# Kernel optimization log

Hardware: AMD Instinct MI355X
Metric: run time of the kernel (lower is better)

## Reference

```python
import jax, jax.numpy as jnp
import numpy as np

N = 30000      # num nodes (cells)
E = 480000     # num edges (avg degree 16)
D_IN = 1000    # input_dim (genes)
H = 8          # nheads
F_H = 32       # hidden_dim per head
D_EMB = 64     # embedding_dim
NEG_SLOPE = 0.2


def setup_inputs() -> dict:
    key = jax.random.key(0)
    ks = jax.random.split(key, 12)
    glorot = lambda k, shape, fan: (jax.random.normal(k, shape, jnp.float32)
                                    * (1.0 / np.sqrt(fan)))
    return {
        "x": jax.random.normal(ks[0], (N, D_IN), jnp.float32),
        "edge_index": jax.random.randint(ks[1], (2, E), 0, N),
        "edge_weight": jax.random.uniform(ks[2], (E,), jnp.float32),
        # GATConv params
        "W": glorot(ks[3], (D_IN, H * F_H), D_IN),
        "att_src": glorot(ks[4], (H, F_H), F_H),
        "att_dst": glorot(ks[5], (H, F_H), F_H),
        "bias_gat": jnp.zeros((H * F_H,), jnp.float32),
        # embedding Linear
        "emb_W": glorot(ks[6], (H * F_H, D_EMB), H * F_H),
        "emb_b": jnp.zeros((D_EMB,), jnp.float32),
        # decoder MLP
        "dec_W1": glorot(ks[7], (D_EMB, F_H), D_EMB),
        "dec_b1": jnp.zeros((F_H,), jnp.float32),
        "dec_W2": glorot(ks[8], (F_H, D_IN), F_H),
        "dec_b2": jnp.zeros((D_IN,), jnp.float32),
    }


def _gat_conv(x, edge_index, W, att_src, att_dst, bias):
    n = x.shape[0]
    h = (x @ W).reshape(n, H, F_H)                    # [N,H,F]
    a_s = jnp.einsum('nhf,hf->nh', h, att_src)        # [N,H]
    a_d = jnp.einsum('nhf,hf->nh', h, att_dst)        # [N,H]
    # add self loops (PyG default add_self_loops=True)
    loops = jnp.arange(n)
    src = jnp.concatenate([edge_index[0], loops])     # [E+N]
    dst = jnp.concatenate([edge_index[1], loops])     # [E+N]
    logits = jax.nn.leaky_relu(a_s[src] + a_d[dst], NEG_SLOPE)  # [E+N,H]
    # segment softmax over incoming edges of each destination node
    m = jax.ops.segment_max(logits, dst, num_segments=n)        # [N,H]
    p = jnp.exp(logits - m[dst])
    denom = jax.ops.segment_sum(p, dst, num_segments=n)         # [N,H]
    alpha = p / denom[dst]                                      # [E+N,H]
    msg = h[src] * alpha[:, :, None]                            # [E+N,H,F]
    out = jax.ops.segment_sum(msg, dst, num_segments=n)         # [N,H,F]
    return out.reshape(n, H * F_H) + bias


def reference(x, edge_index, edge_weight, W, att_src, att_dst, bias_gat,
              emb_W, emb_b, dec_W1, dec_b1, dec_W2, dec_b2):
    # edge_weight is accepted but unused: PyG GATConv with edge_dim=None has
    # no edge-feature pathway.
    h = jax.nn.relu(_gat_conv(x, edge_index, W, att_src, att_dst, bias_gat))
    z = h @ emb_W + emb_b                               # [N, D_EMB]
    d = jax.nn.relu(z @ dec_W1 + dec_b1)                # [N, F_H]
    recon = d @ dec_W2 + dec_b2                         # [N, D_IN]
    return recon, z
```

## Files before the change

### kernel.cpp

```cpp
#include <hip/hip_runtime.h>
#include <hip/hip_bf16.h>

#define N_NODES 30000
#define N_EDGES 480000
#define D_IN    1000
#define KPAD    1024
#define NHEAD   8
#define F_HID   32
#define D_EMB   64
#define NEG_SLOPE 0.2f
#define MAXDEG  64

typedef __attribute__((ext_vector_type(4))) float  f32x4;
typedef __attribute__((ext_vector_type(8))) __bf16 bf16x8;
typedef __attribute__((ext_vector_type(4))) __bf16 bf16x4;

#define WT_TOT    (256*KPAD + D_EMB*256 + F_HID*D_EMB + D_IN*F_HID)
#define WT_BLOCKS ((WT_TOT + 255) / 256)
#define ZC_BLOCKS ((N_NODES + 255) / 256)

__global__ __launch_bounds__(256) void cvt_w(
    const float* __restrict__ W, const float* __restrict__ emb_W,
    const float* __restrict__ d1, const float* __restrict__ d2,
    __bf16* __restrict__ WbT, __bf16* __restrict__ embT,
    __bf16* __restrict__ d1T, __bf16* __restrict__ d2T, int* __restrict__ cnt)
{
    int b = blockIdx.x;
    if (b < WT_BLOCKS) {
        int i = b * 256 + threadIdx.x;
        if (i < 256 * KPAD) {
            int n = i >> 10, k = i & 1023;
            WbT[i] = (k < D_IN) ? (__bf16)W[(size_t)k * 256 + n] : (__bf16)0.0f;
            return;
        }
        i -= 256 * KPAD;
        if (i < D_EMB * 256) {
            int n = i >> 8, k = i & 255;
            embT[i] = (__bf16)emb_W[(size_t)k * D_EMB + n];
            return;
        }
        i -= D_EMB * 256;
        if (i < F_HID * D_EMB) {
            int n = i >> 6, k = i & 63;
            d1T[i] = (__bf16)d1[(size_t)k * F_HID + n];
            return;
        }
        i -= F_HID * D_EMB;
        if (i < D_IN * F_HID) {
            int n = i >> 5, k = i & 31;
            d2T[i] = (__bf16)d2[(size_t)k * D_IN + n];
        }
        return;
    }
    b -= WT_BLOCKS;
    {
        int i = b * 256 + threadIdx.x;
        if (i < N_NODES) cnt[i] = 0;
    }
}

__device__ __forceinline__ void stage_tile(
    __bf16* lds, const __bf16* __restrict__ g, int base, int maxr,
    int K, int k0, int rows, int w, int lane)
{
    const int rsub = lane >> 2;
    const int c    = lane & 3;
    for (int off = w * 1024; off < rows * 64; off += 4096) {
        int r  = (off >> 6) + rsub;
        int gr = base + r; gr = gr > maxr ? maxr : gr;
        int chunk = c ^ (r & 3);
        const __bf16* gp = g + (size_t)gr * K + k0 + chunk * 8;
        __builtin_amdgcn_global_load_lds(
            (const __attribute__((address_space(1))) void*)gp,
            (__attribute__((address_space(3))) void*)((char*)lds + off),
            16, 0, 0);
    }
}

template<int BM, int BN, int RELU>
__global__ __launch_bounds__(256) void gemm_bf16(
    const __bf16* __restrict__ A, const __bf16* __restrict__ Bt,
    float* __restrict__ Cf, __bf16* __restrict__ Cb,
    const float* __restrict__ bias, int M, int Nn, int K)
{
    constexpr int MT = BM / 32;
    constexpr int NT = BN / 32;
    __shared__ __align__(16) __bf16 As[BM * 32];
    __shared__ __align__(16) __bf16 Bs[BN * 32];

    const int tid  = threadIdx.x;
    const int w    = tid >> 6, lane = tid & 63;
    const int wm   = w >> 1,   wn   = w & 1;
    const int quad = lane >> 4, l16 = lane & 15;
    const int bm = blockIdx.x * BM, bn = blockIdx.y * BN;

    f32x4 acc[MT][NT];
    #pragma unroll
    for (int i = 0; i < MT; i++)
        #pragma unroll
        for (int j = 0; j < NT; j++)
            acc[i][j] = (f32x4){0.f, 0.f, 0.f, 0.f};

    for (int k0 = 0; k0 < K; k0 += 32) {
        stage_tile(As, A,  bm, M  - 1, K, k0, BM, w, lane);
        stage_tile(Bs, Bt, bn, Nn - 1, K, k0, BN, w, lane);
        __syncthreads();

        bf16x8 af[MT], bfr[NT];
        #pragma unroll
        for (int mt = 0; mt < MT; mt++) {
            int r = wm * 64 + mt * 16 + l16;
            af[mt] = *(const bf16x8*)&As[r * 32 + (quad ^ (r & 3)) * 8];
        }
        #pragma unroll
        for (int nt = 0; nt < NT; nt++) {
            int r = wn * (NT * 16) + nt * 16 + l16;
            bfr[nt] = *(const bf16x8*)&Bs[r * 32 + (quad ^ (r & 3)) * 8];
        }
        #pragma unroll
        for (int mt = 0; mt < MT; mt++)
            #pragma unroll
            for (int nt = 0; nt < NT; nt++)
                acc[mt][nt] = __builtin_amdgcn_mfma_f32_16x16x32_bf16(
                    af[mt], bfr[nt], acc[mt][nt], 0, 0, 0);
        __syncthreads();
    }

    #pragma unroll
    for (int nt = 0; nt < NT; nt++) {
        int col = bn + wn * (NT * 16) + nt * 16 + l16;
        if (col >= Nn) continue;
        float bv = bias ? bias[col] : 0.0f;
        #pragma unroll
        for (int mt = 0; mt < MT; mt++) {
            int row0 = bm + wm * 64 + mt * 16 + quad * 4;
            #pragma unroll
            for (int rr = 0; rr < 4; rr++) {
                int row = row0 + rr;
                if (row < M) {
                    float v = acc[mt][nt][rr] + bv;
                    if (RELU) v = v > 0.f ? v : 0.f;
                    if (Cf) Cf[(size_t)row * Nn + col] = v;
                    if (Cb) Cb[(size_t)row * Nn + col] = (__bf16)v;
                }
            }
        }
    }
}

__device__ __forceinline__ void a_load_f32(
    const float* __restrict__ x, int bm, int M, int r0, int cb, f32x4* regs)
{
    if (cb < D_IN) {
        int g0 = bm + r0;      g0 = g0 > M - 1 ? M - 1 : g0;
        int g1 = bm + r0 + 64; g1 = g1 > M - 1 ? M - 1 : g1;
        const f32x4* p0 = (const f32x4*)(x + (size_t)g0 * D_IN + cb);
        const f32x4* p1 = (const f32x4*)(x + (size_t)g1 * D_IN + cb);
        regs[0] = p0[0]; regs[1] = p0[1];
        regs[2] = p1[0]; regs[3] = p1[1];
    } else {
        regs[0] = regs[1] = regs[2] = regs[3] = (f32x4){0.f, 0.f, 0.f, 0.f};
    }
}

__global__ __launch_bounds__(256, 1) void gemm1_fused(
    const float* __restrict__ x, const __bf16* __restrict__ WbT,
    __bf16* __restrict__ hb, int M)
{
    __shared__ __align__(16) __bf16 As[128 * 32];
    __shared__ __align__(16) __bf16 Bs[256 * 32];

    const int tid  = threadIdx.x;
    const int w    = tid >> 6, lane = tid & 63;
    const int wm   = w >> 1,   wn   = w & 1;
    const int quad = lane >> 4, l16 = lane & 15;
    const int bm   = blockIdx.x * 128;

    const int r0   = tid >> 2;
    const int cpos = tid & 3;
    const int cxor = (cpos ^ (r0 & 3)) << 3;

    f32x4 acc[4][8];
    #pragma unroll
    for (int i = 0; i < 4; i++)
        #pragma unroll
        for (int j = 0; j < 8; j++)
            acc[i][j] = (f32x4){0.f, 0.f, 0.f, 0.f};

    f32x4 ca[4], na[4];
    a_load_f32(x, bm, M, r0, cxor, ca);

    for (int k0 = 0; k0 < KPAD; k0 += 32) {
        a_load_f32(x, bm, M, r0, (k0 + 32) + cxor, na);
        stage_tile(Bs, WbT, 0, 255, KPAD, k0, 256, w, lane);
        {
            bf16x8 o;
            o[0]=(__bf16)ca[0].x; o[1]=(__bf16)ca[0].y; o[2]=(__bf16)ca[0].z; o[3]=(__bf16)ca[0].w;
            o[4]=(__bf16)ca[1].x; o[5]=(__bf16)ca[1].y; o[6]=(__bf16)ca[1].z; o[7]=(__bf16)ca[1].w;
            *(bf16x8*)&As[r0 * 32 + cpos * 8] = o;
            o[0]=(__bf16)ca[2].x; o[1]=(__bf16)ca[2].y; o[2]=(__bf16)ca[2].z; o[3]=(__bf16)ca[2].w;
            o[4]=(__bf16)ca[3].x; o[5]=(__bf16)ca[3].y; o[6]=(__bf16)ca[3].z; o[7]=(__bf16)ca[3].w;
            *(bf16x8*)&As[(r0 + 64) * 32 + cpos * 8] = o;
        }
        __syncthreads();

        bf16x8 af[4], bfr[8];
        #pragma unroll
        for (int mt = 0; mt < 4; mt++) {
            int r = wm * 64 + mt * 16 + l16;
            af[mt] = *(const bf16x8*)&As[r * 32 + (quad ^ (r & 3)) * 8];
        }
        #pragma unroll
        for (int nt = 0; nt < 8; nt++) {
            int r = wn * 128 + nt * 16 + l16;
            bfr[nt] = *(const bf16x8*)&Bs[r * 32 + (quad ^ (r & 3)) * 8];
        }
        #pragma unroll
        for (int mt = 0; mt < 4; mt++)
            #pragma unroll
            for (int nt = 0; nt < 8; nt++)
                acc[mt][nt] = __builtin_amdgcn_mfma_f32_16x16x32_bf16(
                    af[mt], bfr[nt], acc[mt][nt], 0, 0, 0);
        __syncthreads();

        #pragma unroll
        for (int i = 0; i < 4; i++) ca[i] = na[i];
    }

    #pragma unroll
    for (int nt = 0; nt < 8; nt++) {
        int col = wn * 128 + nt * 16 + l16;
        #pragma unroll
        for (int mt = 0; mt < 4; mt++) {
            int row0 = bm + wm * 64 + mt * 16 + quad * 4;
            #pragma unroll
            for (int rr = 0; rr < 4; rr++) {
                int row = row0 + rr;
                if (row < M)
                    hb[(size_t)row * 256 + col] = (__bf16)acc[mt][nt][rr];
            }
        }
    }
}

#define ATT_BLOCKS ((N_NODES * NHEAD + 255) / 256)
#define SC_BLOCKS  ((N_EDGES + 255) / 256)

__global__ __launch_bounds__(256) void att_scatter(
    const __bf16* __restrict__ hb, const float* __restrict__ att_src,
    const float* __restrict__ att_dst, const int* __restrict__ eidx,
    float* __restrict__ a_s, float* __restrict__ a_d,
    int* __restrict__ cnt, int* __restrict__ slots)
{
    int b = blockIdx.x;
    if (b < ATT_BLOCKS) {
        int i = b * 256 + threadIdx.x;
        if (i >= N_NODES * NHEAD) return;
        int hh = i & 7;
        const bf16x8* hp = (const bf16x8*)(hb + (size_t)i * F_HID);
        const float* sp = att_src + hh * F_HID;
        const float* dp = att_dst + hh * F_HID;
        float s = 0.f, d = 0.f;
        #pragma unroll
        for (int j = 0; j < 4; j++) {
            bf16x8 hv = hp[j];
            #pragma unroll
            for (int t = 0; t < 8; t++) {
                float f = (float)hv[t];
                s += f * sp[j * 8 + t];
                d += f * dp[j * 8 + t];
            }
        }
        a_s[i] = s;
        a_d[i] = d;
        return;
    }
    b -= ATT_BLOCKS;
    {
        int e = b * 256 + threadIdx.x;
        if (e < N_EDGES) {
            int d = eidx[N_EDGES + e];
            int slot = atomicAdd(&cnt[d], 1);
            slots[d * MAXDEG + slot] = eidx[e];
        }
    }
}

__device__ __forceinline__ float leaky(float x) {
    return x > 0.f ? x : NEG_SLOPE * x;
}

__global__ __launch_bounds__(256) void gat_aggregate(
    const __bf16* __restrict__ hb, const float* __restrict__ a_s,
    const float* __restrict__ a_d, const int* __restrict__ cnt,
    const int* __restrict__ slots, const float* __restrict__ bias,
    __bf16* __restrict__ hgatb)
{
    const int wid  = threadIdx.x >> 6;
    const int lane = threadIdx.x & 63;
    const int n = blockIdx.x * 4 + wid;
    if (n >= N_NODES) return;

    const int hh = lane >> 3;
    const int fo = (lane & 7) * 4;
    const int base = n * MAXDEG;
    const int c = cnt[n];
    const float adn = a_d[n * NHEAD + hh];

    float p = __expf(leaky(a_s[n * NHEAD + hh] + adn));
    float denom = p;
    f32x4 acc;
    {
        bf16x4 hv = *(const bf16x4*)(hb + (size_t)n * 256 + hh * F_HID + fo);
        acc.x = p * (float)hv[0]; acc.y = p * (float)hv[1];
        acc.z = p * (float)hv[2]; acc.w = p * (float)hv[3];
    }
    int e = 0;
    for (; e + 4 <= c; e += 4) {
        int s0 = slots[base + e + 0];
        int s1 = slots[base + e + 1];
        int s2 = slots[base + e + 2];
        int s3 = slots[base + e + 3];
        float l0 = a_s[s0 * NHEAD + hh], l1 = a_s[s1 * NHEAD + hh];
        float l2 = a_s[s2 * NHEAD + hh], l3 = a_s[s3 * NHEAD + hh];
        bf16x4 h0 = *(const bf16x4*)(hb + (size_t)s0 * 256 + hh * F_HID + fo);
        bf16x4 h1 = *(const bf16x4*)(hb + (size_t)s1 * 256 + hh * F_HID + fo);
        bf16x4 h2 = *(const bf16x4*)(hb + (size_t)s2 * 256 + hh * F_HID + fo);
        bf16x4 h3 = *(const bf16x4*)(hb + (size_t)s3 * 256 + hh * F_HID + fo);
        float p0 = __expf(leaky(l0 + adn)), p1 = __expf(leaky(l1 + adn));
        float p2 = __expf(leaky(l2 + adn)), p3 = __expf(leaky(l3 + adn));
        denom += (p0 + p1) + (p2 + p3);
        acc.x += p0*(float)h0[0] + p1*(float)h1[0] + p2*(float)h2[0] + p3*(float)h3[0];
        acc.y += p0*(float)h0[1] + p1*(float)h1[1] + p2*(float)h2[1] + p3*(float)h3[1];
        acc.z += p0*(float)h0[2] + p1*(float)h1[2] + p2*(float)h2[2] + p3*(float)h3[2];
        acc.w += p0*(float)h0[3] + p1*(float)h1[3] + p2*(float)h2[3] + p3*(float)h3[3];
    }
    for (; e < c; e++) {
        int s = slots[base + e];
        float pe = __expf(leaky(a_s[s * NHEAD + hh] + adn));
        denom += pe;
        bf16x4 hv = *(const bf16x4*)(hb + (size_t)s * 256 + hh * F_HID + fo);
        acc.x += pe * (float)hv[0]; acc.y += pe * (float)hv[1];
        acc.z += pe * (float)hv[2]; acc.w += pe * (float)hv[3];
    }
    float inv = 1.0f / denom;
    f32x4 bv = *(const f32x4*)(bias + lane * 4);
    float o0 = acc.x * inv + bv.x, o1 = acc.y * inv + bv.y;
    float o2 = acc.z * inv + bv.z, o3 = acc.w * inv + bv.w;
    o0 = o0 > 0.f ? o0 : 0.f;
    o1 = o1 > 0.f ? o1 : 0.f;
    o2 = o2 > 0.f ? o2 : 0.f;
    o3 = o3 > 0.f ? o3 : 0.f;
    bf16x4 ob;
    ob[0] = (__bf16)o0; ob[1] = (__bf16)o1; ob[2] = (__bf16)o2; ob[3] = (__bf16)o3;
    *(bf16x4*)(hgatb + (size_t)n * 256 + lane * 4) = ob;
}

__global__ __launch_bounds__(256) void gemm_zd(
    const __bf16* __restrict__ hgatb, const __bf16* __restrict__ embT,
    const __bf16* __restrict__ d1T, const float* __restrict__ emb_b,
    const float* __restrict__ dec_b1, float* __restrict__ z,
    __bf16* __restrict__ dbufb, int M)
{
    __shared__ __align__(16) __bf16 As[128 * 32];
    __shared__ __align__(16) __bf16 Bs[64 * 32];
    __shared__ __align__(16) __bf16 zS[128 * 64];
    __shared__ __align__(16) __bf16 Bs2[2 * 32 * 32];

    const int tid  = threadIdx.x;
    const int w    = tid >> 6, lane = tid & 63;
    const int wm   = w >> 1,   wn   = w & 1;
    const int quad = lane >> 4, l16 = lane & 15;
    const int bm = blockIdx.x * 128;

    stage_tile(Bs2,        d1T, 0, 31, 64, 0,  32, w, lane);
    stage_tile(Bs2 + 1024, d1T, 0, 31, 64, 32, 32, w, lane);

    f32x4 acc[4][2];
    #pragma unroll
    for (int i = 0; i < 4; i++) { acc[i][0] = (f32x4){0,0,0,0}; acc[i][1] = (f32x4){0,0,0,0}; }

    for (int k0 = 0; k0 < 256; k0 += 32) {
        stage_tile(As, hgatb, bm, M - 1, 256, k0, 128, w, lane);
        stage_tile(Bs, embT,  0,  D_EMB - 1, 256, k0, 64, w, lane);
        __syncthreads();
        bf16x8 af[4], bfr[2];
        #pragma unroll
        for (int mt = 0; mt < 4; mt++) {
            int r = wm * 64 + mt * 16 + l16;
            af[mt] = *(const bf16x8*)&As[r * 32 + (quad ^ (r & 3)) * 8];
        }
        #pragma unroll
        for (int nt = 0; nt < 2; nt++) {
            int r = wn * 32 + nt * 16 + l16;
            bfr[nt] = *(const bf16x8*)&Bs[r * 32 + (quad ^ (r & 3)) * 8];
        }
        #pragma unroll
        for (int mt = 0; mt < 4; mt++)
            #pragma unroll
            for (int nt = 0; nt < 2; nt++)
                acc[mt][nt] = __builtin_amdgcn_mfma_f32_16x16x32_bf16(
                    af[mt], bfr[nt], acc[mt][nt], 0, 0, 0);
        __syncthreads();
    }

    #pragma unroll
    for (int nt = 0; nt < 2; nt++) {
        int col = wn * 32 + nt * 16 + l16;
        float bv = emb_b[col];
        int t = col >> 5, cch = (col >> 3) & 3, j = col & 7;
        #pragma unroll
        for (int mt = 0; mt < 4; mt++) {
            int rl0 = wm * 64 + mt * 16 + quad * 4;
            #pragma unroll
            for (int rr = 0; rr < 4; rr++) {
                int rl = rl0 + rr;
                int row = bm + rl;
                float v = acc[mt][nt][rr] + bv;
                if (row < M) z[(size_t)row * D_EMB + col] = v;
                zS[t * 4096 + rl * 32 + (cch ^ (rl & 3)) * 8 + j] = (__bf16)v;
            }
        }
    }
    __syncthreads();

    f32x4 accd[4];
    #pragma unroll
    for (int i = 0; i < 4; i++) accd[i] = (f32x4){0,0,0,0};
    #pragma unroll
    for (int t = 0; t < 2; t++) {
        bf16x8 af[4], bfr;
        #pragma unroll
        for (int mt = 0; mt < 4; mt++) {
            int r = wm * 64 + mt * 16 + l16;
            af[mt] = *(const bf16x8*)&zS[t * 4096 + r * 32 + (quad ^ (r & 3)) * 8];
        }
        {
            int r = wn * 16 + l16;
            bfr = *(const bf16x8*)&Bs2[t * 1024 + r * 32 + (quad ^ (r & 3)) * 8];
        }
        #pragma unroll
        for (int mt = 0; mt < 4; mt++)
            accd[mt] = __builtin_amdgcn_mfma_f32_16x16x32_bf16(af[mt], bfr, accd[mt], 0, 0, 0);
    }
    {
        int col = wn * 16 + l16;
        float bv = dec_b1[col];
        #pragma unroll
        for (int mt = 0; mt < 4; mt++) {
            int rl0 = wm * 64 + mt * 16 + quad * 4;
            #pragma unroll
            for (int rr = 0; rr < 4; rr++) {
                int row = bm + rl0 + rr;
                if (row < M) {
                    float v = accd[mt][rr] + bv;
                    v = v > 0.f ? v : 0.f;
                    dbufb[(size_t)row * F_HID + col] = (__bf16)v;
                }
            }
        }
    }
}

extern "C" void kernel_launch(void* const* d_in, const int* in_sizes, int n_in,
                              void* d_out, int out_size, void* d_ws, size_t ws_size,
                              hipStream_t stream)
{
    const float* x        = (const float*)d_in[0];
    const int*   eidx     = (const int*)  d_in[1];
    const float* W        = (const float*)d_in[3];
    const float* att_src  = (const float*)d_in[4];
    const float* att_dst  = (const float*)d_in[5];
    const float* bias_gat = (const float*)d_in[6];
    const float* emb_W    = (const float*)d_in[7];
    const float* emb_b    = (const float*)d_in[8];
    const float* dec_W1   = (const float*)d_in[9];
    const float* dec_b1   = (const float*)d_in[10];
    const float* dec_W2   = (const float*)d_in[11];
    const float* dec_b2   = (const float*)d_in[12];

    float* out   = (float*)d_out;
    float* recon = out;
    float* z     = out + (size_t)N_NODES * D_IN;

    char* ws = (char*)d_ws;
    size_t o = 0;
    auto alloc = [&](size_t bytes) { char* p = ws + o; o = (o + bytes + 255) & ~(size_t)255; return p; };
    __bf16* hb      = (__bf16*)alloc((size_t)N_NODES * 256 * 2);
    __bf16* WbT     = (__bf16*)alloc((size_t)256 * KPAD * 2);
    __bf16* embT    = (__bf16*)alloc((size_t)D_EMB * 256 * 2);
    __bf16* d1T     = (__bf16*)alloc((size_t)F_HID * D_EMB * 2);
    __bf16* d2T     = (__bf16*)alloc((size_t)D_IN * F_HID * 2);
    __bf16* hgatb   = (__bf16*)alloc((size_t)N_NODES * 256 * 2);
    __bf16* dbufb   = (__bf16*)alloc((size_t)N_NODES * F_HID * 2);
    float*  a_s     = (float*) alloc((size_t)N_NODES * NHEAD * 4);
    float*  a_d     = (float*) alloc((size_t)N_NODES * NHEAD * 4);
    int*    slots   = (int*)   alloc((size_t)N_NODES * MAXDEG * 4);
    int*    cnt     = (int*)   alloc((size_t)N_NODES * 4);

    const int MB = (N_NODES + 127) / 128;

    cvt_w<<<WT_BLOCKS + ZC_BLOCKS, 256, 0, stream>>>(
        W, emb_W, dec_W1, dec_W2, WbT, embT, d1T, d2T, cnt);

    gemm1_fused<<<MB, 256, 0, stream>>>(x, WbT, hb, N_NODES);

    att_scatter<<<ATT_BLOCKS + SC_BLOCKS, 256, 0, stream>>>(
        hb, att_src, att_dst, eidx, a_s, a_d, cnt, slots);

    gat_aggregate<<<N_NODES / 4, 256, 0, stream>>>(
        hb, a_s, a_d, cnt, slots, bias_gat, hgatb);

    gemm_zd<<<MB, 256, 0, stream>>>(
        hgatb, embT, d1T, emb_b, dec_b1, z, dbufb, N_NODES);

    gemm_bf16<128, 128, 0><<<dim3(MB, 8), 256, 0, stream>>>(
        dbufb, d2T, recon, (__bf16*)nullptr, dec_b2, N_NODES, D_IN, F_HID);
}
```

Measured before the change: 419.7 us.

## Fold attention projections into GEMM1 and double-buffer with 512-thread blocks

Precomputes W·att_src and W·att_dst as an extra 16-column bf16 weight, so GEMM1 produces the per-head attention logits a_s/a_d through extra MFMAs and the separate att pass over h is gone. GEMM1 moves to 512 threads with double-buffered LDS tiles, so global loads of the next K slice overlap compute. Edge scatter becomes its own kernel and the aggregate reads neighbour slots as int4. Logits now come from bf16-rounded x times bf16-rounded fused weights instead of from bf16 h, which changes numerics slightly, and the doubled LDS and larger blocks change occupancy.

```diff
diff --git a/kernel.cpp b/kernel.cpp
--- a/kernel.cpp
+++ b/kernel.cpp
@@ -17,13 +17,16 @@
 
 #define WT_TOT    (256*KPAD + D_EMB*256 + F_HID*D_EMB + D_IN*F_HID)
 #define WT_BLOCKS ((WT_TOT + 255) / 256)
+#define WA_BLOCKS (16 * KPAD / 256)
 #define ZC_BLOCKS ((N_NODES + 255) / 256)
 
 __global__ __launch_bounds__(256) void cvt_w(
     const float* __restrict__ W, const float* __restrict__ emb_W,
     const float* __restrict__ d1, const float* __restrict__ d2,
+    const float* __restrict__ att_src, const float* __restrict__ att_dst,
     __bf16* __restrict__ WbT, __bf16* __restrict__ embT,
-    __bf16* __restrict__ d1T, __bf16* __restrict__ d2T, int* __restrict__ cnt)
+    __bf16* __restrict__ d1T, __bf16* __restrict__ d2T,
+    __bf16* __restrict__ WaT, int* __restrict__ cnt)
 {
     int b = blockIdx.x;
     if (b < WT_BLOCKS) {
@@ -53,19 +56,46 @@
         return;
     }
     b -= WT_BLOCKS;
+    if (b < WA_BLOCKS) {
+        int i = b * 256 + threadIdx.x;
+        int j = i >> 10, k = i & 1023;
+        float s = 0.f;
+        if (k < D_IN) {
+            const float* av = (j < 8 ? att_src : att_dst) + (j & 7) * F_HID;
+            const float* wr = W + (size_t)k * 256 + (j & 7) * F_HID;
+            #pragma unroll
+            for (int f = 0; f < F_HID; f++) s += wr[f] * av[f];
+        }
+        WaT[i] = (__bf16)s;
+        return;
+    }
+    b -= WA_BLOCKS;
     {
         int i = b * 256 + threadIdx.x;
         if (i < N_NODES) cnt[i] = 0;
     }
 }
 
+#define SC_BLOCKS  ((N_EDGES + 255) / 256)
+
+__global__ __launch_bounds__(256) void edge_scatter(
+    const int* __restrict__ eidx, int* __restrict__ cnt, int* __restrict__ slots)
+{
+    int e = blockIdx.x * 256 + threadIdx.x;
+    if (e < N_EDGES) {
+        int d = eidx[N_EDGES + e];
+        int slot = atomicAdd(&cnt[d], 1);
+        slots[d * MAXDEG + slot] = eidx[e];
+    }
+}
+
 __device__ __forceinline__ void stage_tile(
     __bf16* lds, const __bf16* __restrict__ g, int base, int maxr,
-    int K, int k0, int rows, int w, int lane)
+    int K, int k0, int rows, int w, int lane, int stride)
 {
     const int rsub = lane >> 2;
     const int c    = lane & 3;
-    for (int off = w * 1024; off < rows * 64; off += 4096) {
+    for (int off = w * 1024; off < rows * 64; off += stride) {
         int r  = (off >> 6) + rsub;
         int gr = base + r; gr = gr > maxr ? maxr : gr;
         int chunk = c ^ (r & 3);
@@ -102,8 +132,8 @@
             acc[i][j] = (f32x4){0.f, 0.f, 0.f, 0.f};
 
     for (int k0 = 0; k0 < K; k0 += 32) {
-        stage_tile(As, A,  bm, M  - 1, K, k0, BM, w, lane);
-        stage_tile(Bs, Bt, bn, Nn - 1, K, k0, BN, w, lane);
+        stage_tile(As, A,  bm, M  - 1, K, k0, BM, w, lane, 4096);
+        stage_tile(Bs, Bt, bn, Nn - 1, K, k0, BN, w, lane, 4096);
         __syncthreads();
 
         bf16x8 af[MT], bfr[NT];
@@ -148,88 +178,133 @@
     }
 }
 
-__device__ __forceinline__ void a_load_f32(
-    const float* __restrict__ x, int bm, int M, int r0, int cb, f32x4* regs)
+__device__ __forceinline__ void xload8(const float* __restrict__ xrow, int cb,
+                                       f32x4& u0, f32x4& u1)
 {
     if (cb < D_IN) {
-        int g0 = bm + r0;      g0 = g0 > M - 1 ? M - 1 : g0;
-        int g1 = bm + r0 + 64; g1 = g1 > M - 1 ? M - 1 : g1;
-        const f32x4* p0 = (const f32x4*)(x + (size_t)g0 * D_IN + cb);
-        const f32x4* p1 = (const f32x4*)(x + (size_t)g1 * D_IN + cb);
-        regs[0] = p0[0]; regs[1] = p0[1];
-        regs[2] = p1[0]; regs[3] = p1[1];
+        const f32x4* p = (const f32x4*)(xrow + cb);
+        u0 = p[0]; u1 = p[1];
     } else {
-        regs[0] = regs[1] = regs[2] = regs[3] = (f32x4){0.f, 0.f, 0.f, 0.f};
-    }
-}
-
-__global__ __launch_bounds__(256, 1) void gemm1_fused(
+        u0 = (f32x4){0.f, 0.f, 0.f, 0.f};
+        u1 = (f32x4){0.f, 0.f, 0.f, 0.f};
+    }
+}
+
+__device__ __forceinline__ bf16x8 cvt8(const f32x4& u0, const f32x4& u1)
+{
+    bf16x8 o;
+    o[0] = (__bf16)u0.x; o[1] = (__bf16)u0.y; o[2] = (__bf16)u0.z; o[3] = (__bf16)u0.w;
+    o[4] = (__bf16)u1.x; o[5] = (__bf16)u1.y; o[6] = (__bf16)u1.z; o[7] = (__bf16)u1.w;
+    return o;
+}
+
+__global__ __launch_bounds__(512, 2) void gemm1_fused(
     const float* __restrict__ x, const __bf16* __restrict__ WbT,
-    __bf16* __restrict__ hb, int M)
-{
-    __shared__ __align__(16) __bf16 As[128 * 32];
-    __shared__ __align__(16) __bf16 Bs[256 * 32];
+    const __bf16* __restrict__ WaT, __bf16* __restrict__ hb,
+    float* __restrict__ a_s, float* __restrict__ a_d, int M)
+{
+    __shared__ __align__(16) __bf16 As[2][128 * 32];
+    __shared__ __align__(16) __bf16 Bs[2][256 * 32];
 
     const int tid  = threadIdx.x;
     const int w    = tid >> 6, lane = tid & 63;
-    const int wm   = w >> 1,   wn   = w & 1;
+    const int wm   = w >> 2,   wn   = w & 3;
     const int quad = lane >> 4, l16 = lane & 15;
     const int bm   = blockIdx.x * 128;
 
     const int r0   = tid >> 2;
     const int cpos = tid & 3;
     const int cxor = (cpos ^ (r0 & 3)) << 3;
-
-    f32x4 acc[4][8];
+    int grow = bm + r0; if (grow > M - 1) grow = M - 1;
+    const float* xrow = x + (size_t)grow * D_IN;
+
+    const int brsub = lane >> 2;
+    const int bc    = lane & 3;
+
+    f32x4 acc[4][4];
     #pragma unroll
     for (int i = 0; i < 4; i++)
         #pragma unroll
-        for (int j = 0; j < 8; j++)
+        for (int j = 0; j < 4; j++)
             acc[i][j] = (f32x4){0.f, 0.f, 0.f, 0.f};
-
-    f32x4 ca[4], na[4];
-    a_load_f32(x, bm, M, r0, cxor, ca);
-
-    for (int k0 = 0; k0 < KPAD; k0 += 32) {
-        a_load_f32(x, bm, M, r0, (k0 + 32) + cxor, na);
-        stage_tile(Bs, WbT, 0, 255, KPAD, k0, 256, w, lane);
-        {
-            bf16x8 o;
-            o[0]=(__bf16)ca[0].x; o[1]=(__bf16)ca[0].y; o[2]=(__bf16)ca[0].z; o[3]=(__bf16)ca[0].w;
-            o[4]=(__bf16)ca[1].x; o[5]=(__bf16)ca[1].y; o[6]=(__bf16)ca[1].z; o[7]=(__bf16)ca[1].w;
-            *(bf16x8*)&As[r0 * 32 + cpos * 8] = o;
-            o[0]=(__bf16)ca[2].x; o[1]=(__bf16)ca[2].y; o[2]=(__bf16)ca[2].z; o[3]=(__bf16)ca[2].w;
-            o[4]=(__bf16)ca[3].x; o[5]=(__bf16)ca[3].y; o[6]=(__bf16)ca[3].z; o[7]=(__bf16)ca[3].w;
-            *(bf16x8*)&As[(r0 + 64) * 32 + cpos * 8] = o;
-        }
-        __syncthreads();
-
-        bf16x8 af[4], bfr[8];
+    f32x4 accA[4];
+    #pragma unroll
+    for (int i = 0; i < 4; i++) accA[i] = (f32x4){0.f, 0.f, 0.f, 0.f};
+
+    const bool att = (wn == 0);
+    const __bf16* warow = WaT + (size_t)l16 * KPAD + quad * 8;
+
+    auto stageB = [&](int buf, int k0) {
+        #pragma unroll
+        for (int off = 0; off < 16384; off += 8192) {
+            int o2 = off + w * 1024;
+            int r = (o2 >> 6) + brsub;
+            int chunk = bc ^ (r & 3);
+            const __bf16* gp = WbT + (size_t)r * KPAD + k0 + chunk * 8;
+            __builtin_amdgcn_global_load_lds(
+                (const __attribute__((address_space(1))) void*)gp,
+                (__attribute__((address_space(3))) void*)((char*)&Bs[buf][0] + o2),
+                16, 0, 0);
+        }
+    };
+
+    auto compute = [&](int buf, const bf16x8& attfrag) {
+        bf16x8 af[4], bfr[4];
         #pragma unroll
         for (int mt = 0; mt < 4; mt++) {
             int r = wm * 64 + mt * 16 + l16;
-            af[mt] = *(const bf16x8*)&As[r * 32 + (quad ^ (r & 3)) * 8];
-        }
-        #pragma unroll
-        for (int nt = 0; nt < 8; nt++) {
-            int r = wn * 128 + nt * 16 + l16;
-            bfr[nt] = *(const bf16x8*)&Bs[r * 32 + (quad ^ (r & 3)) * 8];
+            af[mt] = *(const bf16x8*)&As[buf][r * 32 + (quad ^ (r & 3)) * 8];
+        }
+        #pragma unroll
+        for (int nt = 0; nt < 4; nt++) {
+            int r = wn * 64 + nt * 16 + l16;
+            bfr[nt] = *(const bf16x8*)&Bs[buf][r * 32 + (quad ^ (r & 3)) * 8];
         }
         #pragma unroll
         for (int mt = 0; mt < 4; mt++)
             #pragma unroll
-            for (int nt = 0; nt < 8; nt++)
+            for (int nt = 0; nt < 4; nt++)
                 acc[mt][nt] = __builtin_amdgcn_mfma_f32_16x16x32_bf16(
                     af[mt], bfr[nt], acc[mt][nt], 0, 0, 0);
+        if (att) {
+            #pragma unroll
+            for (int mt = 0; mt < 4; mt++)
+                accA[mt] = __builtin_amdgcn_mfma_f32_16x16x32_bf16(
+                    af[mt], attfrag, accA[mt], 0, 0, 0);
+        }
+    };
+
+    f32x4 xa0, xa1, xb0, xb1;
+    bf16x8 attEv = {}, attOd = {};
+
+    xload8(xrow, 0 + cxor, xa0, xa1);
+    xload8(xrow, 32 + cxor, xb0, xb1);
+    if (att) attEv = *(const bf16x8*)(warow + 0);
+    *(bf16x8*)&As[0][r0 * 32 + cpos * 8] = cvt8(xa0, xa1);
+    stageB(0, 0);
+    __syncthreads();
+
+    for (int k0 = 0; k0 < KPAD; k0 += 64) {
+        xload8(xrow, (k0 + 64) + cxor, xa0, xa1);
+        if (att) attOd = *(const bf16x8*)(warow + k0 + 32);
+        *(bf16x8*)&As[1][r0 * 32 + cpos * 8] = cvt8(xb0, xb1);
+        stageB(1, k0 + 32);
+        compute(0, attEv);
         __syncthreads();
 
-        #pragma unroll
-        for (int i = 0; i < 4; i++) ca[i] = na[i];
-    }
-
-    #pragma unroll
-    for (int nt = 0; nt < 8; nt++) {
-        int col = wn * 128 + nt * 16 + l16;
+        if (k0 + 64 < KPAD) {
+            xload8(xrow, (k0 + 96) + cxor, xb0, xb1);
+            if (att) attEv = *(const bf16x8*)(warow + k0 + 64);
+            *(bf16x8*)&As[0][r0 * 32 + cpos * 8] = cvt8(xa0, xa1);
+            stageB(0, k0 + 64);
+        }
+        compute(1, attOd);
+        __syncthreads();
+    }
+
+    #pragma unroll
+    for (int nt = 0; nt < 4; nt++) {
+        int col = wn * 64 + nt * 16 + l16;
         #pragma unroll
         for (int mt = 0; mt < 4; mt++) {
             int row0 = bm + wm * 64 + mt * 16 + quad * 4;
@@ -241,47 +316,19 @@
             }
         }
     }
-}
-
-#define ATT_BLOCKS ((N_NODES * NHEAD + 255) / 256)
-#define SC_BLOCKS  ((N_EDGES + 255) / 256)
-
-__global__ __launch_bounds__(256) void att_scatter(
-    const __bf16* __restrict__ hb, const float* __restrict__ att_src,
-    const float* __restrict__ att_dst, const int* __restrict__ eidx,
-    float* __restrict__ a_s, float* __restrict__ a_d,
-    int* __restrict__ cnt, int* __restrict__ slots)
-{
-    int b = blockIdx.x;
-    if (b < ATT_BLOCKS) {
-        int i = b * 256 + threadIdx.x;
-        if (i >= N_NODES * NHEAD) return;
-        int hh = i & 7;
-        const bf16x8* hp = (const bf16x8*)(hb + (size_t)i * F_HID);
-        const float* sp = att_src + hh * F_HID;
-        const float* dp = att_dst + hh * F_HID;
-        float s = 0.f, d = 0.f;
-        #pragma unroll
-        for (int j = 0; j < 4; j++) {
-            bf16x8 hv = hp[j];
-            #pragma unroll
-            for (int t = 0; t < 8; t++) {
-                float f = (float)hv[t];
-                s += f * sp[j * 8 + t];
-                d += f * dp[j * 8 + t];
+    if (att) {
+        #pragma unroll
+        for (int mt = 0; mt < 4; mt++) {
+            int row0 = bm + wm * 64 + mt * 16 + quad * 4;
+            #pragma unroll
+            for (int rr = 0; rr < 4; rr++) {
+                int row = row0 + rr;
+                if (row < M) {
+                    float v = accA[mt][rr];
+                    if (l16 < 8) a_s[row * NHEAD + l16] = v;
+                    else         a_d[row * NHEAD + (l16 - 8)] = v;
+                }
             }
-        }
-        a_s[i] = s;
-        a_d[i] = d;
-        return;
-    }
-    b -= ATT_BLOCKS;
-    {
-        int e = b * 256 + threadIdx.x;
-        if (e < N_EDGES) {
-            int d = eidx[N_EDGES + e];
-            int slot = atomicAdd(&cnt[d], 1);
-            slots[d * MAXDEG + slot] = eidx[e];
         }
     }
 }
@@ -317,10 +364,8 @@
     }
     int e = 0;
     for (; e + 4 <= c; e += 4) {
-        int s0 = slots[base + e + 0];
-        int s1 = slots[base + e + 1];
-        int s2 = slots[base + e + 2];
-        int s3 = slots[base + e + 3];
+        const int4 ss = *(const int4*)(slots + base + e);
+        int s0 = ss.x, s1 = ss.y, s2 = ss.z, s3 = ss.w;
         float l0 = a_s[s0 * NHEAD + hh], l1 = a_s[s1 * NHEAD + hh];
         float l2 = a_s[s2 * NHEAD + hh], l3 = a_s[s3 * NHEAD + hh];
         bf16x4 h0 = *(const bf16x4*)(hb + (size_t)s0 * 256 + hh * F_HID + fo);
@@ -373,16 +418,16 @@
     const int quad = lane >> 4, l16 = lane & 15;
     const int bm = blockIdx.x * 128;
 
-    stage_tile(Bs2,        d1T, 0, 31, 64, 0,  32, w, lane);
-    stage_tile(Bs2 + 1024, d1T, 0, 31, 64, 32, 32, w, lane);
+    stage_tile(Bs2,        d1T, 0, 31, 64, 0,  32, w, lane, 4096);
+    stage_tile(Bs2 + 1024, d1T, 0, 31, 64, 32, 32, w, lane, 4096);
 
     f32x4 acc[4][2];
     #pragma unroll
     for (int i = 0; i < 4; i++) { acc[i][0] = (f32x4){0,0,0,0}; acc[i][1] = (f32x4){0,0,0,0}; }
 
     for (int k0 = 0; k0 < 256; k0 += 32) {
-        stage_tile(As, hgatb, bm, M - 1, 256, k0, 128, w, lane);
-        stage_tile(Bs, embT,  0,  D_EMB - 1, 256, k0, 64, w, lane);
+        stage_tile(As, hgatb, bm, M - 1, 256, k0, 128, w, lane, 4096);
+        stage_tile(Bs, embT,  0,  D_EMB - 1, 256, k0, 64, w, lane, 4096);
         __syncthreads();
         bf16x8 af[4], bfr[2];
         #pragma unroll
@@ -491,6 +536,7 @@
     __bf16* embT    = (__bf16*)alloc((size_t)D_EMB * 256 * 2);
     __bf16* d1T     = (__bf16*)alloc((size_t)F_HID * D_EMB * 2);
     __bf16* d2T     = (__bf16*)alloc((size_t)D_IN * F_HID * 2);
+    __bf16* WaT     = (__bf16*)alloc((size_t)16 * KPAD * 2);
     __bf16* hgatb   = (__bf16*)alloc((size_t)N_NODES * 256 * 2);
     __bf16* dbufb   = (__bf16*)alloc((size_t)N_NODES * F_HID * 2);
     float*  a_s     = (float*) alloc((size_t)N_NODES * NHEAD * 4);
@@ -500,13 +546,13 @@
 
     const int MB = (N_NODES + 127) / 128;
 
-    cvt_w<<<WT_BLOCKS + ZC_BLOCKS, 256, 0, stream>>>(
-        W, emb_W, dec_W1, dec_W2, WbT, embT, d1T, d2T, cnt);
-
-    gemm1_fused<<<MB, 256, 0, stream>>>(x, WbT, hb, N_NODES);
-
-    att_scatter<<<ATT_BLOCKS + SC_BLOCKS, 256, 0, stream>>>(
-        hb, att_src, att_dst, eidx, a_s, a_d, cnt, slots);
+    cvt_w<<<WT_BLOCKS + WA_BLOCKS + ZC_BLOCKS, 256, 0, stream>>>(
+        W, emb_W, dec_W1, dec_W2, att_src, att_dst,
+        WbT, embT, d1T, d2T, WaT, cnt);
+
+    edge_scatter<<<SC_BLOCKS, 256, 0, stream>>>(eidx, cnt, slots);
+
+    gemm1_fused<<<MB, 512, 0, stream>>>(x, WbT, WaT, hb, a_s, a_d, N_NODES);
 
     gat_aggregate<<<N_NODES / 4, 256, 0, stream>>>(
         hb, a_s, a_d, cnt, slots, bias_gat, hgatb);
```

New measurement: 409.1 us. -2.5%, faster.
